# Performance work log

Hardware: AMD Instinct MI355X
Metric: run time of the kernel (lower is better)

The kernel has to match this reference:

```python
import jax, jax.numpy as jnp
import numpy as np
from jax import lax

EPS = 1e-5

def ste_sign(x):
    # forward-only module: plain sign is fine
    return jnp.sign(x)

def conv2d(x, w, pad):
    # x: NCHW, w: OIHW, stride 1
    return lax.conv_general_dilated(x, w, window_strides=(1, 1),
                                    padding=[(pad, pad), (pad, pad)],
                                    dimension_numbers=('NCHW', 'OIHW', 'NCHW'))

def maxpool2(x):
    # 2x2 max pool, stride 2, VALID (floor) -- matches nn.MaxPool2d(2,2)
    return lax.reduce_window(x, -jnp.inf, lax.max, (1, 1, 2, 2), (1, 1, 2, 2), 'VALID')

def batchnorm(x, gamma, beta):
    # training-mode BN: batch statistics over (N,H,W), biased variance
    mean = jnp.mean(x, axis=(0, 2, 3), keepdims=True)
    var = jnp.var(x, axis=(0, 2, 3), keepdims=True)
    xn = (x - mean) * lax.rsqrt(var + EPS)
    return xn * gamma[None, :, None, None] + beta[None, :, None, None]

def setup_inputs() -> dict:
    key = jax.random.key(0)
    ks = jax.random.split(key, 8)
    def he(k, shape):
        n = shape[2] * shape[3] * shape[0]
        return jax.random.normal(k, shape, jnp.float32) * np.sqrt(2.0 / n)
    x = jax.random.normal(ks[0], (4096, 1, 28, 28), jnp.float32)
    w0 = he(ks[1], (32, 1, 3, 3))
    w1 = he(ks[2], (32, 32, 3, 3))
    w2 = he(ks[3], (32, 32, 3, 3))
    g0 = jnp.ones((32,), jnp.float32); b0 = jnp.zeros((32,), jnp.float32)
    g1 = jnp.ones((32,), jnp.float32); b1 = jnp.zeros((32,), jnp.float32)
    g2 = jnp.ones((32,), jnp.float32); b2 = jnp.zeros((32,), jnp.float32)
    fw = jax.random.normal(ks[4], (10, 288), jnp.float32) * 0.01
    fb = jnp.zeros((10,), jnp.float32)
    return {"x": x, "w0": w0, "g0": g0, "b0": b0, "w1": w1, "g1": g1, "b1": b1,
            "w2": w2, "g2": g2, "b2": b2, "fw": fw, "fb": fb}

def reference(x, w0, g0, b0, w1, g1, b1, w2, g2, b2, fw, fb):
    # block0: fp conv -> pool -> bn (no act)
    h = batchnorm(maxpool2(conv2d(x, w0, 1)), g0, b0)          # [B,32,14,14]
    # block1: binary(1w1a) conv -> pool -> bn + maxpool(shortcut)
    o = batchnorm(maxpool2(conv2d(ste_sign(h), ste_sign(w1), 1)), g1, b1)
    h = o + maxpool2(h)                                         # [B,32,7,7]
    # block2
    o = batchnorm(maxpool2(conv2d(ste_sign(h), ste_sign(w2), 1)), g2, b2)
    h = o + maxpool2(h)                                         # [B,32,3,3]
    h = h.reshape(h.shape[0], -1)                                # [B,288]
    return h @ fw.T + fb                                         # [B,10]
```

## Files before the change

### kernel.cpp

```cpp
#include <hip/hip_runtime.h>
#include <stdint.h>

#define BATCH 4096

typedef float v16f __attribute__((ext_vector_type(16)));
typedef short v8s  __attribute__((ext_vector_type(8)));

__device__ __forceinline__ int sgn8(float v) {
    return (v > 0.f) ? 1 : ((v < 0.f) ? -1 : 0);
}

__global__ __launch_bounds__(448) void k_conv0s(const float* __restrict__ x,
                                                const float* __restrict__ w0,
                                                const float* __restrict__ w1,
                                                const float* __restrict__ w2,
                                                uint16_t* __restrict__ w1f,
                                                uint16_t* __restrict__ w2f,
                                                double* __restrict__ part0) {
    __shared__ float xs[960];
    __shared__ float wl[288];
    __shared__ double rs[448], rq[448];
    int n = blockIdx.x, t = threadIdx.x;

    if (n < 72 && t < 256) {
        int i = n * 256 + t;
        int ii = (i < 9216) ? i : i - 9216;
        const float* w = (i < 9216) ? w1 : w2;
        uint16_t* o = (i < 9216) ? w1f : w2f;
        int j = ii & 7, nn = (ii >> 3) & 31, q2 = (ii >> 8) & 1, kh = (ii >> 9) & 1, tp = ii >> 10;
        int cin = kh * 16 + q2 * 8 + j;
        float v = w[(nn * 32 + cin) * 9 + tp];
        o[ii] = (v > 0.f) ? 0x3F80 : ((v < 0.f) ? 0xBF80 : 0);
    }

    for (int i = t; i < 960; i += 448) xs[i] = 0.f;
    for (int i = t; i < 288; i += 448) wl[i] = w0[i];
    __syncthreads();
    for (int i = t; i < 784; i += 448) {
        int y = i / 28, xx = i - y * 28;
        xs[(y + 1) * 32 + xx + 1] = x[n * 784 + i];
    }
    __syncthreads();
    int c = t & 31, py = t >> 5;
    float wreg[9];
    #pragma unroll
    for (int i = 0; i < 9; ++i) wreg[i] = wl[c * 9 + i];
    const float4* X4 = (const float4*)xs;
    float4 cur0 = X4[(2 * py + 0) * 8];
    float4 cur1 = X4[(2 * py + 1) * 8];
    float4 cur2 = X4[(2 * py + 2) * 8];
    float4 cur3 = X4[(2 * py + 3) * 8];
    double s = 0.0, q = 0.0;
    #pragma unroll
    for (int k = 0; k < 7; ++k) {
        float4 n0 = X4[(2 * py + 0) * 8 + k + 1];
        float4 n1 = X4[(2 * py + 1) * 8 + k + 1];
        float4 n2 = X4[(2 * py + 2) * 8 + k + 1];
        float4 n3 = X4[(2 * py + 3) * 8 + k + 1];
        float a[4][6];
        a[0][0] = cur0.x; a[0][1] = cur0.y; a[0][2] = cur0.z; a[0][3] = cur0.w; a[0][4] = n0.x; a[0][5] = n0.y;
        a[1][0] = cur1.x; a[1][1] = cur1.y; a[1][2] = cur1.z; a[1][3] = cur1.w; a[1][4] = n1.x; a[1][5] = n1.y;
        a[2][0] = cur2.x; a[2][1] = cur2.y; a[2][2] = cur2.z; a[2][3] = cur2.w; a[2][4] = n2.x; a[2][5] = n2.y;
        a[3][0] = cur3.x; a[3][1] = cur3.y; a[3][2] = cur3.z; a[3][3] = cur3.w; a[3][4] = n3.x; a[3][5] = n3.y;
        #pragma unroll
        for (int e = 0; e < 2; ++e) {
            int base = 2 * e;
            float s00 = 0.f, s01 = 0.f, s10 = 0.f, s11 = 0.f;
            #pragma unroll
            for (int ky = 0; ky < 3; ++ky)
            #pragma unroll
            for (int kx = 0; kx < 3; ++kx) {
                float w = wreg[ky * 3 + kx];
                s00 = fmaf(a[ky][base + kx], w, s00);
                s01 = fmaf(a[ky][base + kx + 1], w, s01);
                s10 = fmaf(a[ky + 1][base + kx], w, s10);
                s11 = fmaf(a[ky + 1][base + kx + 1], w, s11);
            }
            float m = fmaxf(fmaxf(s00, s01), fmaxf(s10, s11));
            double v = (double)m;
            s += v; q += v * v;
        }
        cur0 = n0; cur1 = n1; cur2 = n2; cur3 = n3;
    }
    rs[c * 14 + py] = s; rq[c * 14 + py] = q;
    __syncthreads();
    if (t < 32) {
        double S = 0.0, Q = 0.0;
        #pragma unroll
        for (int i = 0; i < 14; ++i) { S += rs[t * 14 + i]; Q += rq[t * 14 + i]; }
        part0[(size_t)t * 4096 + n] = S;
        part0[(size_t)32 * 4096 + (size_t)t * 4096 + n] = Q;
    }
}

__global__ __launch_bounds__(256) void k_finalize(const double* __restrict__ part, int G,
                                                  const float* __restrict__ g,
                                                  const float* __restrict__ b,
                                                  double inv_count, float* __restrict__ ss) {
    int c = blockIdx.x, t = threadIdx.x;
    double s = 0.0, q = 0.0;
    for (int i = t; i < G; i += 256) {
        s += part[(size_t)c * G + i];
        q += part[(size_t)32 * G + (size_t)c * G + i];
    }
    #pragma unroll
    for (int o = 32; o > 0; o >>= 1) { s += __shfl_down(s, o); q += __shfl_down(q, o); }
    __shared__ double rs[4], rq[4];
    int w = t >> 6, l = t & 63;
    if (l == 0) { rs[w] = s; rq[w] = q; }
    __syncthreads();
    if (t == 0) {
        s = rs[0] + rs[1] + rs[2] + rs[3];
        q = rq[0] + rq[1] + rq[2] + rq[3];
        double mean = s * inv_count;
        double var = q * inv_count - mean * mean;
        double sc = (double)g[c] / sqrt(var + 1e-5);
        ss[c] = (float)sc;
        ss[32 + c] = (float)((double)b[c] - mean * sc);
    }
}

__global__ __launch_bounds__(448) void k_bn0r(const float* __restrict__ x,
                                              const float* __restrict__ w0,
                                              const float* __restrict__ ss,
                                              uint32_t* __restrict__ s0b,
                                              float* __restrict__ hp0) {
    __shared__ float xs[960];
    __shared__ float wl[288];
    __shared__ float P[6468];
    int n = blockIdx.x, t = threadIdx.x;
    for (int i = t; i < 960; i += 448) xs[i] = 0.f;
    for (int i = t; i < 288; i += 448) wl[i] = w0[i];
    __syncthreads();
    for (int i = t; i < 784; i += 448) {
        int y = i / 28, xx = i - y * 28;
        xs[(y + 1) * 32 + xx + 1] = x[n * 784 + i];
    }
    __syncthreads();
    int c = t & 31, py = t >> 5;
    float wreg[9];
    #pragma unroll
    for (int i = 0; i < 9; ++i) wreg[i] = wl[c * 9 + i];
    float sc = ss[c], sh = ss[32 + c];
    const float4* X4 = (const float4*)xs;
    float4 cur0 = X4[(2 * py + 0) * 8];
    float4 cur1 = X4[(2 * py + 1) * 8];
    float4 cur2 = X4[(2 * py + 2) * 8];
    float4 cur3 = X4[(2 * py + 3) * 8];
    #pragma unroll
    for (int k = 0; k < 7; ++k) {
        float4 n0 = X4[(2 * py + 0) * 8 + k + 1];
        float4 n1 = X4[(2 * py + 1) * 8 + k + 1];
        float4 n2 = X4[(2 * py + 2) * 8 + k + 1];
        float4 n3 = X4[(2 * py + 3) * 8 + k + 1];
        float a[4][6];
        a[0][0] = cur0.x; a[0][1] = cur0.y; a[0][2] = cur0.z; a[0][3] = cur0.w; a[0][4] = n0.x; a[0][5] = n0.y;
        a[1][0] = cur1.x; a[1][1] = cur1.y; a[1][2] = cur1.z; a[1][3] = cur1.w; a[1][4] = n1.x; a[1][5] = n1.y;
        a[2][0] = cur2.x; a[2][1] = cur2.y; a[2][2] = cur2.z; a[2][3] = cur2.w; a[2][4] = n2.x; a[2][5] = n2.y;
        a[3][0] = cur3.x; a[3][1] = cur3.y; a[3][2] = cur3.z; a[3][3] = cur3.w; a[3][4] = n3.x; a[3][5] = n3.y;
        #pragma unroll
        for (int e = 0; e < 2; ++e) {
            int base = 2 * e;
            float s00 = 0.f, s01 = 0.f, s10 = 0.f, s11 = 0.f;
            #pragma unroll
            for (int ky = 0; ky < 3; ++ky)
            #pragma unroll
            for (int kx = 0; kx < 3; ++kx) {
                float w = wreg[ky * 3 + kx];
                s00 = fmaf(a[ky][base + kx], w, s00);
                s01 = fmaf(a[ky][base + kx + 1], w, s01);
                s10 = fmaf(a[ky + 1][base + kx], w, s10);
                s11 = fmaf(a[ky + 1][base + kx + 1], w, s11);
            }
            float m = fmaxf(fmaxf(s00, s01), fmaxf(s10, s11));
            P[(py * 14 + 2 * k + e) * 33 + c] = fmaf(sc, m, sh);
        }
        cur0 = n0; cur1 = n1; cur2 = n2; cur3 = n3;
    }
    __syncthreads();
    uint32_t* simg = s0b + (size_t)n * 4096;
    for (int i = t; i < 784; i += 448) {
        int pl = i >> 2, qd = i & 3;
        int iy = pl / 14, ix = pl - iy * 14;
        int yy = iy + 1, xx2 = ix + 1;
        int p = yy * 16 + xx2;
        int psw = (xx2 & 3) ^ (yy & 3);
        int g = qd ^ psw;
        const float* Pp = &P[pl * 33 + g * 8];
        uint32_t d[4];
        #pragma unroll
        for (int j = 0; j < 4; ++j) {
            float h0 = Pp[2 * j], h1 = Pp[2 * j + 1];
            uint32_t b0 = (h0 > 0.f) ? 0x3F80u : ((h0 < 0.f) ? 0xBF80u : 0u);
            uint32_t b1 = (h1 > 0.f) ? 0x3F80u : ((h1 < 0.f) ? 0xBF80u : 0u);
            d[j] = b0 | (b1 << 16);
        }
        uint4 v; v.x = d[0]; v.y = d[1]; v.z = d[2]; v.w = d[3];
        *(uint4*)(simg + p * 16 + qd * 4) = v;
    }
    if (t < 240) {
        int e = t >> 2, qd = t & 3;
        int yh, xh;
        if (e < 16)      { yh = 0;      xh = e; }
        else if (e < 32) { yh = 15;     xh = e - 16; }
        else if (e < 46) { yh = e - 31; xh = 0; }
        else             { yh = e - 45; xh = 15; }
        uint4 z; z.x = z.y = z.z = z.w = 0u;
        *(uint4*)(simg + (yh * 16 + xh) * 16 + qd * 4) = z;
    }
    if (t < 196) {
        int pw = t >> 2, oct = t & 3;
        int pyy = pw / 7, pxx = pw - pyy * 7;
        int b00 = ((2 * pyy) * 14 + 2 * pxx) * 33;
        int b01 = b00 + 33;
        int b10 = b00 + 14 * 33;
        int b11 = b10 + 33;
        float out[8];
        #pragma unroll
        for (int k = 0; k < 8; ++k) {
            int cc = oct * 8 + k;
            out[k] = fmaxf(fmaxf(P[b00 + cc], P[b01 + cc]),
                           fmaxf(P[b10 + cc], P[b11 + cc]));
        }
        float4* hd = (float4*)(hp0 + ((size_t)n * 49 + pw) * 32 + oct * 8);
        float4 h0; h0.x = out[0]; h0.y = out[1]; h0.z = out[2]; h0.w = out[3];
        float4 h1; h1.x = out[4]; h1.y = out[5]; h1.z = out[6]; h1.w = out[7];
        hd[0] = h0; hd[1] = h1;
    }
}

__global__ __launch_bounds__(256) void k_conv1m(const uint32_t* __restrict__ s0b,
                                                const uint16_t* __restrict__ w1f,
                                                float* __restrict__ p1,
                                                double* __restrict__ part1) {
    __shared__ uint32_t lds[8192];
    int t = threadIdx.x;
    int n0 = blockIdx.x * 2;
    const uint4* gp = (const uint4*)(s0b + (size_t)n0 * 4096);
    uint4* lp = (uint4*)lds;
    #pragma unroll
    for (int i = 0; i < 8; ++i) lp[t + i * 256] = gp[t + i * 256];
    int lane = t & 63, wv = t >> 6;
    int q = lane >> 5, ncol = lane & 31;
    v8s wfr[18];
    #pragma unroll
    for (int f = 0; f < 18; ++f)
        wfr[f] = *(const v8s*)(w1f + (f * 2 + q) * 256 + ncol * 8);
    __syncthreads();
    int img = wv >> 1, wh = wv & 1;
    int n = n0 + img;
    int ibase = img * 4096;
    int m = lane & 31;
    int quad = m & 3, pwl = m >> 2;
    int dy = quad >> 1, dx = quad & 1;
    double sAcc = 0.0, qAcc = 0.0;
    for (int tile = wh; tile < 7; tile += 2) {
        int pw = tile * 8 + pwl;
        int pwc = min(pw, 48);
        int py = pwc / 7, px = pwc - py * 7;
        int pbase = (2 * py + dy) * 16 + 2 * px + dx;
        v16f acc;
        #pragma unroll
        for (int i = 0; i < 16; ++i) acc[i] = 0.f;
        #pragma unroll
        for (int tp = 0; tp < 9; ++tp) {
            int p = pbase + (tp / 3) * 16 + (tp % 3);
            int psw = (p ^ (p >> 4)) & 3;
            #pragma unroll
            for (int kh = 0; kh < 2; ++kh) {
                int g = kh * 2 + q;
                int idx = ibase + p * 16 + ((g ^ psw) << 2);
                v8s a = *(const v8s*)&lds[idx];
                acc = __builtin_amdgcn_mfma_f32_32x32x16_bf16(a, wfr[tp * 2 + kh], acc, 0, 0, 0);
            }
        }
        #pragma unroll
        for (int g4 = 0; g4 < 4; ++g4) {
            float mx = fmaxf(fmaxf(acc[4 * g4], acc[4 * g4 + 1]),
                             fmaxf(acc[4 * g4 + 2], acc[4 * g4 + 3]));
            int pwo = tile * 8 + 2 * g4 + q;
            if (pwo < 49) {
                p1[((size_t)n * 49 + pwo) * 32 + ncol] = mx;
                double v = (double)mx;
                sAcc += v; qAcc += v * v;
            }
        }
    }
    __syncthreads();
    double* red = (double*)lds;
    red[(wv * 2 + q) * 32 + ncol] = sAcc;
    red[256 + (wv * 2 + q) * 32 + ncol] = qAcc;
    __syncthreads();
    if (t < 32) {
        double S = 0.0, Q = 0.0;
        #pragma unroll
        for (int i = 0; i < 8; ++i) { S += red[i * 32 + t]; Q += red[256 + i * 32 + t]; }
        part1[(size_t)t * 2048 + blockIdx.x] = S;
        part1[(size_t)32 * 2048 + (size_t)t * 2048 + blockIdx.x] = Q;
    }
}

__global__ __launch_bounds__(256) void k_bc2m(const float* __restrict__ p1,
                                              const float* __restrict__ hp0,
                                              const float* __restrict__ ss,
                                              const uint16_t* __restrict__ w2f,
                                              float* __restrict__ p2,
                                              float* __restrict__ hp1,
                                              double* __restrict__ part2) {
    __shared__ uint32_t lds[8192];
    __shared__ float Htmp[1568];
    int t = threadIdx.x;
    int n0 = blockIdx.x * 8;
    int lane = t & 63, wv = t >> 6;
    int q = lane >> 5, ncol = lane & 31;
    v8s wfr[18];
    #pragma unroll
    for (int f = 0; f < 18; ++f)
        wfr[f] = *(const v8s*)(w2f + (f * 2 + q) * 256 + ncol * 8);

    int cbase = (t & 7) * 4;
    float sc4[4], sh4[4];
    #pragma unroll
    for (int j = 0; j < 4; ++j) { sc4[j] = ss[64 + cbase + j]; sh4[j] = ss[96 + cbase + j]; }

    float4 pa, pb, ha, hb;
    {
        const float4* P4 = (const float4*)(p1 + (size_t)n0 * 1568);
        const float4* H4 = (const float4*)(hp0 + (size_t)n0 * 1568);
        pa = P4[t]; ha = H4[t];
        if (t < 136) { pb = P4[256 + t]; hb = H4[256 + t]; }
    }

    float4* Ht4 = (float4*)Htmp;
    for (int img = 0; img < 8; ++img) {
        float4 npa, npb, nha, nhb;
        if (img < 7) {
            const float4* P4 = (const float4*)(p1 + (size_t)(n0 + img + 1) * 1568);
            const float4* H4 = (const float4*)(hp0 + (size_t)(n0 + img + 1) * 1568);
            npa = P4[t]; nha = H4[t];
            if (t < 136) { npb = P4[256 + t]; nhb = H4[256 + t]; }
        }
        if (img) __syncthreads();
        {
            float4 hv;
            hv.x = fmaf(sc4[0], pa.x, sh4[0]) + ha.x;
            hv.y = fmaf(sc4[1], pa.y, sh4[1]) + ha.y;
            hv.z = fmaf(sc4[2], pa.z, sh4[2]) + ha.z;
            hv.w = fmaf(sc4[3], pa.w, sh4[3]) + ha.w;
            Ht4[t] = hv;
            if (t < 136) {
                float4 hw;
                hw.x = fmaf(sc4[0], pb.x, sh4[0]) + hb.x;
                hw.y = fmaf(sc4[1], pb.y, sh4[1]) + hb.y;
                hw.z = fmaf(sc4[2], pb.z, sh4[2]) + hb.z;
                hw.w = fmaf(sc4[3], pb.w, sh4[3]) + hb.w;
                Ht4[256 + t] = hw;
            }
        }
        __syncthreads();
        uint32_t* ap = &lds[img * 1024];
        #pragma unroll
        for (int ii = 0; ii < 4; ++ii) {
            int i = t + ii * 256;
            int pp = i >> 4, r = i & 15;
            int y = pp >> 3, xq = pp & 7;
            uint32_t d = 0u;
            if (y >= 1 && xq >= 1) {
                int pix = (y - 1) * 7 + (xq - 1);
                int sub = r & 3;
                int g = (r >> 2) ^ (pp & 3);
                int c0 = ((g << 2) | sub) * 2;
                float h0 = Htmp[pix * 32 + c0];
                float h1 = Htmp[pix * 32 + c0 + 1];
                uint32_t b0 = (h0 > 0.f) ? 0x3F80u : ((h0 < 0.f) ? 0xBF80u : 0u);
                uint32_t b1 = (h1 > 0.f) ? 0x3F80u : ((h1 < 0.f) ? 0xBF80u : 0u);
                d = b0 | (b1 << 16);
            }
            ap[i] = d;
        }
        for (int jj = t; jj < 288; jj += 256) {
            int c = jj / 9, pix = jj - c * 9;
            int r = pix / 3, qq = pix - r * 3;
            float a0 = Htmp[((2 * r) * 7 + 2 * qq) * 32 + c];
            float a1 = Htmp[((2 * r) * 7 + 2 * qq + 1) * 32 + c];
            float a2 = Htmp[((2 * r + 1) * 7 + 2 * qq) * 32 + c];
            float a3 = Htmp[((2 * r + 1) * 7 + 2 * qq + 1) * 32 + c];
            hp1[(size_t)(n0 + img) * 288 + c * 9 + pix] = fmaxf(fmaxf(a0, a1), fmaxf(a2, a3));
        }
        pa = npa; pb = npb; ha = nha; hb = nhb;
    }
    __syncthreads();

    int m = lane & 31;
    int quad = m & 3, pwl = m >> 2;
    int dy = quad >> 1, dx = quad & 1;
    double sAcc = 0.0, qAcc = 0.0;
    for (int tile = wv; tile < 9; tile += 4) {
        int pwg = tile * 8 + pwl;
        int img = pwg / 9, pwi = pwg - img * 9;
        int py = pwi / 3, px = pwi - py * 3;
        int pbase = (2 * py + dy) * 8 + 2 * px + dx;
        v16f acc;
        #pragma unroll
        for (int i = 0; i < 16; ++i) acc[i] = 0.f;
        #pragma unroll
        for (int tp = 0; tp < 9; ++tp) {
            int p = pbase + (tp / 3) * 8 + (tp % 3);
            int psw = p & 3;
            #pragma unroll
            for (int kh = 0; kh < 2; ++kh) {
                int g = kh * 2 + q;
                int idx = img * 1024 + p * 16 + ((g ^ psw) << 2);
                v8s a = *(const v8s*)&lds[idx];
                acc = __builtin_amdgcn_mfma_f32_32x32x16_bf16(a, wfr[tp * 2 + kh], acc, 0, 0, 0);
            }
        }
        #pragma unroll
        for (int g4 = 0; g4 < 4; ++g4) {
            float mx = fmaxf(fmaxf(acc[4 * g4], acc[4 * g4 + 1]),
                             fmaxf(acc[4 * g4 + 2], acc[4 * g4 + 3]));
            int pwo = tile * 8 + 2 * g4 + q;
            int oimg = pwo / 9, opwi = pwo - oimg * 9;
            p2[(size_t)(n0 + oimg) * 288 + ncol * 9 + opwi] = mx;
            double v = (double)mx;
            sAcc += v; qAcc += v * v;
        }
    }
    __syncthreads();
    double* red = (double*)lds;
    red[(wv * 2 + q) * 32 + ncol] = sAcc;
    red[256 + (wv * 2 + q) * 32 + ncol] = qAcc;
    __syncthreads();
    if (t < 32) {
        double S = 0.0, Q = 0.0;
        #pragma unroll
        for (int i = 0; i < 8; ++i) { S += red[i * 32 + t]; Q += red[256 + i * 32 + t]; }
        part2[(size_t)t * 512 + blockIdx.x] = S;
        part2[(size_t)32 * 512 + (size_t)t * 512 + blockIdx.x] = Q;
    }
}

__global__ __launch_bounds__(256) void k_fc(const float* __restrict__ p2,
                                            const float* __restrict__ hp1,
                                            const float* __restrict__ ss,
                                            const float* __restrict__ fw,
                                            const float* __restrict__ fb,
                                            float* __restrict__ outv) {
    int wv = threadIdx.x >> 6, l = threadIdx.x & 63;
    int n = blockIdx.x * 4 + wv;
    float acc[10];
    #pragma unroll
    for (int k = 0; k < 10; ++k) acc[k] = 0.f;
    #pragma unroll
    for (int i = 0; i < 5; ++i) {
        int j = l + 64 * i;
        if (j < 288) {
            int c = j / 9;
            float h = fmaf(ss[128 + c], p2[n * 288 + j], ss[160 + c]) + hp1[n * 288 + j];
            #pragma unroll
            for (int k = 0; k < 10; ++k)
                acc[k] = fmaf(h, fw[k * 288 + j], acc[k]);
        }
    }
    #pragma unroll
    for (int k = 0; k < 10; ++k) {
        float s = acc[k];
        #pragma unroll
        for (int o = 32; o > 0; o >>= 1) s += __shfl_down(s, o);
        if (l == 0) outv[n * 10 + k] = s + fb[k];
    }
}

extern "C" void kernel_launch(void* const* d_in, const int* in_sizes, int n_in,
                              void* d_out, int out_size, void* d_ws, size_t ws_size,
                              hipStream_t stream) {
    (void)in_sizes; (void)n_in; (void)out_size; (void)ws_size;
    const float* x  = (const float*)d_in[0];
    const float* w0 = (const float*)d_in[1];
    const float* g0 = (const float*)d_in[2];
    const float* b0 = (const float*)d_in[3];
    const float* w1 = (const float*)d_in[4];
    const float* g1 = (const float*)d_in[5];
    const float* b1 = (const float*)d_in[6];
    const float* w2 = (const float*)d_in[7];
    const float* g2 = (const float*)d_in[8];
    const float* b2 = (const float*)d_in[9];
    const float* fw = (const float*)d_in[10];
    const float* fb = (const float*)d_in[11];
    float* outv = (float*)d_out;
    char* ws = (char*)d_ws;

    float*     ss    = (float*)(ws + 1024);
    uint16_t*  w1f   = (uint16_t*)(ws + 2048);
    uint16_t*  w2f   = (uint16_t*)(ws + 38912);
    float*     p1    = (float*)(ws + 76800);
    float*     hp1   = (float*)(ws + 32582656);
    float*     p2    = (float*)(ws + 37301248);
    uint32_t*  s0b   = (uint32_t*)(ws + 42019840);
    double*    part0 = (double*)(ws + 109128704);
    double*    part1 = (double*)(ws + 111225856);
    double*    part2 = (double*)(ws + 112274432);
    float*     hp0   = (float*)(ws + 128527360);

    k_conv0s<<<BATCH, 448, 0, stream>>>(x, w0, w1, w2, w1f, w2f, part0);
    k_finalize<<<32, 256, 0, stream>>>(part0, 4096, g0, b0, 1.0 / (BATCH * 196.0), ss);
    k_bn0r<<<BATCH, 448, 0, stream>>>(x, w0, ss, s0b, hp0);

    k_conv1m<<<BATCH / 2, 256, 0, stream>>>(s0b, w1f, p1, part1);
    k_finalize<<<32, 256, 0, stream>>>(part1, 2048, g1, b1, 1.0 / (BATCH * 49.0), ss + 64);

    k_bc2m<<<BATCH / 8, 256, 0, stream>>>(p1, hp0, ss, w2f, p2, hp1, part2);
    k_finalize<<<32, 256, 0, stream>>>(part2, 512, g2, b2, 1.0 / (BATCH * 9.0), ss + 128);

    k_fc<<<BATCH / 4, 256, 0, stream>>>(p2, hp1, ss, fw, fb, outv);
}
```

Baseline: 203.8 us.

## Store pooled conv0 output once and fold BN0 into downstream kernels

```diff
diff --git a/kernel.cpp b/kernel.cpp
--- a/kernel.cpp
+++ b/kernel.cpp
@@ -6,17 +6,14 @@
 typedef float v16f __attribute__((ext_vector_type(16)));
 typedef short v8s  __attribute__((ext_vector_type(8)));
 
-__device__ __forceinline__ int sgn8(float v) {
-    return (v > 0.f) ? 1 : ((v < 0.f) ? -1 : 0);
-}
-
-__global__ __launch_bounds__(448) void k_conv0s(const float* __restrict__ x,
+__global__ __launch_bounds__(448) void k_conv0f(const float* __restrict__ x,
                                                 const float* __restrict__ w0,
                                                 const float* __restrict__ w1,
                                                 const float* __restrict__ w2,
                                                 uint16_t* __restrict__ w1f,
                                                 uint16_t* __restrict__ w2f,
-                                                double* __restrict__ part0) {
+                                                double* __restrict__ part0,
+                                                float* __restrict__ mg) {
     __shared__ float xs[960];
     __shared__ float wl[288];
     __shared__ double rs[448], rq[448];
@@ -50,6 +47,7 @@
     float4 cur1 = X4[(2 * py + 1) * 8];
     float4 cur2 = X4[(2 * py + 2) * 8];
     float4 cur3 = X4[(2 * py + 3) * 8];
+    float* mrow = mg + (size_t)n * 6272;
     double s = 0.0, q = 0.0;
     #pragma unroll
     for (int k = 0; k < 7; ++k) {
@@ -77,6 +75,8 @@
                 s11 = fmaf(a[ky + 1][base + kx + 1], w, s11);
             }
             float m = fmaxf(fmaxf(s00, s01), fmaxf(s10, s11));
+            int pix = py * 14 + 2 * k + e;
+            mrow[pix * 32 + c] = m;
             double v = (double)m;
             s += v; q += v * v;
         }
@@ -120,138 +120,70 @@
     }
 }
 
-__global__ __launch_bounds__(448) void k_bn0r(const float* __restrict__ x,
-                                              const float* __restrict__ w0,
-                                              const float* __restrict__ ss,
-                                              uint32_t* __restrict__ s0b,
-                                              float* __restrict__ hp0) {
-    __shared__ float xs[960];
-    __shared__ float wl[288];
-    __shared__ float P[6468];
-    int n = blockIdx.x, t = threadIdx.x;
-    for (int i = t; i < 960; i += 448) xs[i] = 0.f;
-    for (int i = t; i < 288; i += 448) wl[i] = w0[i];
-    __syncthreads();
-    for (int i = t; i < 784; i += 448) {
-        int y = i / 28, xx = i - y * 28;
-        xs[(y + 1) * 32 + xx + 1] = x[n * 784 + i];
-    }
-    __syncthreads();
-    int c = t & 31, py = t >> 5;
-    float wreg[9];
-    #pragma unroll
-    for (int i = 0; i < 9; ++i) wreg[i] = wl[c * 9 + i];
-    float sc = ss[c], sh = ss[32 + c];
-    const float4* X4 = (const float4*)xs;
-    float4 cur0 = X4[(2 * py + 0) * 8];
-    float4 cur1 = X4[(2 * py + 1) * 8];
-    float4 cur2 = X4[(2 * py + 2) * 8];
-    float4 cur3 = X4[(2 * py + 3) * 8];
-    #pragma unroll
-    for (int k = 0; k < 7; ++k) {
-        float4 n0 = X4[(2 * py + 0) * 8 + k + 1];
-        float4 n1 = X4[(2 * py + 1) * 8 + k + 1];
-        float4 n2 = X4[(2 * py + 2) * 8 + k + 1];
-        float4 n3 = X4[(2 * py + 3) * 8 + k + 1];
-        float a[4][6];
-        a[0][0] = cur0.x; a[0][1] = cur0.y; a[0][2] = cur0.z; a[0][3] = cur0.w; a[0][4] = n0.x; a[0][5] = n0.y;
-        a[1][0] = cur1.x; a[1][1] = cur1.y; a[1][2] = cur1.z; a[1][3] = cur1.w; a[1][4] = n1.x; a[1][5] = n1.y;
-        a[2][0] = cur2.x; a[2][1] = cur2.y; a[2][2] = cur2.z; a[2][3] = cur2.w; a[2][4] = n2.x; a[2][5] = n2.y;
-        a[3][0] = cur3.x; a[3][1] = cur3.y; a[3][2] = cur3.z; a[3][3] = cur3.w; a[3][4] = n3.x; a[3][5] = n3.y;
-        #pragma unroll
-        for (int e = 0; e < 2; ++e) {
-            int base = 2 * e;
-            float s00 = 0.f, s01 = 0.f, s10 = 0.f, s11 = 0.f;
-            #pragma unroll
-            for (int ky = 0; ky < 3; ++ky)
-            #pragma unroll
-            for (int kx = 0; kx < 3; ++kx) {
-                float w = wreg[ky * 3 + kx];
-                s00 = fmaf(a[ky][base + kx], w, s00);
-                s01 = fmaf(a[ky][base + kx + 1], w, s01);
-                s10 = fmaf(a[ky + 1][base + kx], w, s10);
-                s11 = fmaf(a[ky + 1][base + kx + 1], w, s11);
-            }
-            float m = fmaxf(fmaxf(s00, s01), fmaxf(s10, s11));
-            P[(py * 14 + 2 * k + e) * 33 + c] = fmaf(sc, m, sh);
-        }
-        cur0 = n0; cur1 = n1; cur2 = n2; cur3 = n3;
-    }
-    __syncthreads();
-    uint32_t* simg = s0b + (size_t)n * 4096;
-    for (int i = t; i < 784; i += 448) {
-        int pl = i >> 2, qd = i & 3;
-        int iy = pl / 14, ix = pl - iy * 14;
-        int yy = iy + 1, xx2 = ix + 1;
-        int p = yy * 16 + xx2;
-        int psw = (xx2 & 3) ^ (yy & 3);
-        int g = qd ^ psw;
-        const float* Pp = &P[pl * 33 + g * 8];
-        uint32_t d[4];
-        #pragma unroll
-        for (int j = 0; j < 4; ++j) {
-            float h0 = Pp[2 * j], h1 = Pp[2 * j + 1];
-            uint32_t b0 = (h0 > 0.f) ? 0x3F80u : ((h0 < 0.f) ? 0xBF80u : 0u);
-            uint32_t b1 = (h1 > 0.f) ? 0x3F80u : ((h1 < 0.f) ? 0xBF80u : 0u);
-            d[j] = b0 | (b1 << 16);
-        }
-        uint4 v; v.x = d[0]; v.y = d[1]; v.z = d[2]; v.w = d[3];
-        *(uint4*)(simg + p * 16 + qd * 4) = v;
-    }
-    if (t < 240) {
-        int e = t >> 2, qd = t & 3;
-        int yh, xh;
-        if (e < 16)      { yh = 0;      xh = e; }
-        else if (e < 32) { yh = 15;     xh = e - 16; }
-        else if (e < 46) { yh = e - 31; xh = 0; }
-        else             { yh = e - 45; xh = 15; }
-        uint4 z; z.x = z.y = z.z = z.w = 0u;
-        *(uint4*)(simg + (yh * 16 + xh) * 16 + qd * 4) = z;
-    }
-    if (t < 196) {
-        int pw = t >> 2, oct = t & 3;
-        int pyy = pw / 7, pxx = pw - pyy * 7;
-        int b00 = ((2 * pyy) * 14 + 2 * pxx) * 33;
-        int b01 = b00 + 33;
-        int b10 = b00 + 14 * 33;
-        int b11 = b10 + 33;
-        float out[8];
-        #pragma unroll
-        for (int k = 0; k < 8; ++k) {
-            int cc = oct * 8 + k;
-            out[k] = fmaxf(fmaxf(P[b00 + cc], P[b01 + cc]),
-                           fmaxf(P[b10 + cc], P[b11 + cc]));
-        }
-        float4* hd = (float4*)(hp0 + ((size_t)n * 49 + pw) * 32 + oct * 8);
-        float4 h0; h0.x = out[0]; h0.y = out[1]; h0.z = out[2]; h0.w = out[3];
-        float4 h1; h1.x = out[4]; h1.y = out[5]; h1.z = out[6]; h1.w = out[7];
-        hd[0] = h0; hd[1] = h1;
-    }
-}
-
-__global__ __launch_bounds__(256) void k_conv1m(const uint32_t* __restrict__ s0b,
+__global__ __launch_bounds__(256) void k_conv1s(const float* __restrict__ m,
+                                                const float* __restrict__ ss,
                                                 const uint16_t* __restrict__ w1f,
                                                 float* __restrict__ p1,
                                                 double* __restrict__ part1) {
     __shared__ uint32_t lds[8192];
     int t = threadIdx.x;
     int n0 = blockIdx.x * 2;
-    const uint4* gp = (const uint4*)(s0b + (size_t)n0 * 4096);
-    uint4* lp = (uint4*)lds;
-    #pragma unroll
-    for (int i = 0; i < 8; ++i) lp[t + i * 256] = gp[t + i * 256];
     int lane = t & 63, wv = t >> 6;
     int q = lane >> 5, ncol = lane & 31;
     v8s wfr[18];
     #pragma unroll
     for (int f = 0; f < 18; ++f)
         wfr[f] = *(const v8s*)(w1f + (f * 2 + q) * 256 + ncol * 8);
-    __syncthreads();
+
+    uint4 z4; z4.x = z4.y = z4.z = z4.w = 0u;
+    for (int i = t; i < 480; i += 256) {
+        int img = (i >= 240) ? 1 : 0;
+        int e2 = i - img * 240;
+        int e = e2 >> 2, qd = e2 & 3;
+        int yh, xh;
+        if (e < 16)      { yh = 0;      xh = e; }
+        else if (e < 32) { yh = 15;     xh = e - 16; }
+        else if (e < 46) { yh = e - 31; xh = 0; }
+        else             { yh = e - 45; xh = 15; }
+        *(uint4*)&lds[img * 4096 + (yh * 16 + xh) * 16 + qd * 4] = z4;
+    }
+    int u = t >> 2, tq = t & 3;
+    float sc8[8], sh8[8];
+    #pragma unroll
+    for (int j = 0; j < 8; ++j) { sc8[j] = ss[tq * 8 + j]; sh8[j] = ss[32 + tq * 8 + j]; }
+    for (int pg = u; pg < 392; pg += 64) {
+        int img = (pg >= 196) ? 1 : 0;
+        int pl = pg - img * 196;
+        int iy = pl / 14, ix = pl - iy * 14;
+        int yy = iy + 1, xx2 = ix + 1;
+        int p = yy * 16 + xx2;
+        int psw = (xx2 & 3) ^ (yy & 3);
+        int qd = tq ^ psw;
+        const float4* mp = (const float4*)(m + ((size_t)(n0 + img) * 196 + pl) * 32 + tq * 8);
+        float4 v0 = mp[0], v1 = mp[1];
+        float h[8];
+        h[0] = fmaf(sc8[0], v0.x, sh8[0]); h[1] = fmaf(sc8[1], v0.y, sh8[1]);
+        h[2] = fmaf(sc8[2], v0.z, sh8[2]); h[3] = fmaf(sc8[3], v0.w, sh8[3]);
+        h[4] = fmaf(sc8[4], v1.x, sh8[4]); h[5] = fmaf(sc8[5], v1.y, sh8[5]);
+        h[6] = fmaf(sc8[6], v1.z, sh8[6]); h[7] = fmaf(sc8[7], v1.w, sh8[7]);
+        uint32_t d[4];
+        #pragma unroll
+        for (int j = 0; j < 4; ++j) {
+            float h0 = h[2 * j], h1 = h[2 * j + 1];
+            uint32_t b0 = (h0 > 0.f) ? 0x3F80u : ((h0 < 0.f) ? 0xBF80u : 0u);
+            uint32_t b1 = (h1 > 0.f) ? 0x3F80u : ((h1 < 0.f) ? 0xBF80u : 0u);
+            d[j] = b0 | (b1 << 16);
+        }
+        uint4 v; v.x = d[0]; v.y = d[1]; v.z = d[2]; v.w = d[3];
+        *(uint4*)&lds[img * 4096 + p * 16 + qd * 4] = v;
+    }
+    __syncthreads();
+
     int img = wv >> 1, wh = wv & 1;
     int n = n0 + img;
     int ibase = img * 4096;
-    int m = lane & 31;
-    int quad = m & 3, pwl = m >> 2;
+    int mm = lane & 31;
+    int quad = mm & 3, pwl = mm >> 2;
     int dy = quad >> 1, dx = quad & 1;
     double sAcc = 0.0, qAcc = 0.0;
     for (int tile = wh; tile < 7; tile += 2) {
@@ -301,7 +233,7 @@
 }
 
 __global__ __launch_bounds__(256) void k_bc2m(const float* __restrict__ p1,
-                                              const float* __restrict__ hp0,
+                                              const float* __restrict__ m,
                                               const float* __restrict__ ss,
                                               const uint16_t* __restrict__ w2f,
                                               float* __restrict__ p2,
@@ -313,47 +245,84 @@
     int n0 = blockIdx.x * 8;
     int lane = t & 63, wv = t >> 6;
     int q = lane >> 5, ncol = lane & 31;
-    v8s wfr[18];
-    #pragma unroll
-    for (int f = 0; f < 18; ++f)
-        wfr[f] = *(const v8s*)(w2f + (f * 2 + q) * 256 + ncol * 8);
-
-    int cbase = (t & 7) * 4;
-    float sc4[4], sh4[4];
-    #pragma unroll
-    for (int j = 0; j < 4; ++j) { sc4[j] = ss[64 + cbase + j]; sh4[j] = ss[96 + cbase + j]; }
-
-    float4 pa, pb, ha, hb;
+
+    int cb = t & 7;
+    float sc1v[4], sh1v[4], sc0v[4], sh0v[4];
+    #pragma unroll
+    for (int j = 0; j < 4; ++j) {
+        sc1v[j] = ss[64 + cb * 4 + j]; sh1v[j] = ss[96 + cb * 4 + j];
+        sc0v[j] = ss[cb * 4 + j];      sh0v[j] = ss[32 + cb * 4 + j];
+    }
+    int pw0 = t >> 3;
+    int py0 = pw0 / 7, px0 = pw0 - py0 * 7;
+    int mb0 = ((2 * py0) * 14 + 2 * px0) * 8 + cb;
+    int pw1 = 32 + (t >> 3);
+    int py1 = pw1 / 7, px1 = pw1 - py1 * 7;
+    int mb1 = ((2 * py1) * 14 + 2 * px1) * 8 + cb;
+
+    float4 pa, pb, a0, a1, a2, a3, b0_, b1_, b2_, b3_;
     {
         const float4* P4 = (const float4*)(p1 + (size_t)n0 * 1568);
-        const float4* H4 = (const float4*)(hp0 + (size_t)n0 * 1568);
-        pa = P4[t]; ha = H4[t];
-        if (t < 136) { pb = P4[256 + t]; hb = H4[256 + t]; }
+        const float4* M4 = (const float4*)(m + (size_t)n0 * 6272);
+        pa = P4[t];
+        a0 = M4[mb0]; a1 = M4[mb0 + 8]; a2 = M4[mb0 + 112]; a3 = M4[mb0 + 120];
+        if (t < 136) {
+            pb = P4[256 + t];
+            b0_ = M4[mb1]; b1_ = M4[mb1 + 8]; b2_ = M4[mb1 + 112]; b3_ = M4[mb1 + 120];
+        }
     }
 
     float4* Ht4 = (float4*)Htmp;
     for (int img = 0; img < 8; ++img) {
-        float4 npa, npb, nha, nhb;
+        float4 npa, npb, na0, na1, na2, na3, nb0, nb1, nb2, nb3;
         if (img < 7) {
             const float4* P4 = (const float4*)(p1 + (size_t)(n0 + img + 1) * 1568);
-            const float4* H4 = (const float4*)(hp0 + (size_t)(n0 + img + 1) * 1568);
-            npa = P4[t]; nha = H4[t];
-            if (t < 136) { npb = P4[256 + t]; nhb = H4[256 + t]; }
+            const float4* M4 = (const float4*)(m + (size_t)(n0 + img + 1) * 6272);
+            npa = P4[t];
+            na0 = M4[mb0]; na1 = M4[mb0 + 8]; na2 = M4[mb0 + 112]; na3 = M4[mb0 + 120];
+            if (t < 136) {
+                npb = P4[256 + t];
+                nb0 = M4[mb1]; nb1 = M4[mb1 + 8]; nb2 = M4[mb1 + 112]; nb3 = M4[mb1 + 120];
+            }
         }
         if (img) __syncthreads();
         {
+            float mx0 = fmaxf(fmaxf(a0.x, a1.x), fmaxf(a2.x, a3.x));
+            float mx1 = fmaxf(fmaxf(a0.y, a1.y), fmaxf(a2.y, a3.y));
+            float mx2 = fmaxf(fmaxf(a0.z, a1.z), fmaxf(a2.z, a3.z));
+            float mx3 = fmaxf(fmaxf(a0.w, a1.w), fmaxf(a2.w, a3.w));
+            float mn0 = fminf(fminf(a0.x, a1.x), fminf(a2.x, a3.x));
+            float mn1 = fminf(fminf(a0.y, a1.y), fminf(a2.y, a3.y));
+            float mn2 = fminf(fminf(a0.z, a1.z), fminf(a2.z, a3.z));
+            float mn3 = fminf(fminf(a0.w, a1.w), fminf(a2.w, a3.w));
+            float s0 = (sc0v[0] > 0.f) ? mx0 : mn0;
+            float s1 = (sc0v[1] > 0.f) ? mx1 : mn1;
+            float s2 = (sc0v[2] > 0.f) ? mx2 : mn2;
+            float s3 = (sc0v[3] > 0.f) ? mx3 : mn3;
             float4 hv;
-            hv.x = fmaf(sc4[0], pa.x, sh4[0]) + ha.x;
-            hv.y = fmaf(sc4[1], pa.y, sh4[1]) + ha.y;
-            hv.z = fmaf(sc4[2], pa.z, sh4[2]) + ha.z;
-            hv.w = fmaf(sc4[3], pa.w, sh4[3]) + ha.w;
+            hv.x = fmaf(sc1v[0], pa.x, sh1v[0]) + fmaf(sc0v[0], s0, sh0v[0]);
+            hv.y = fmaf(sc1v[1], pa.y, sh1v[1]) + fmaf(sc0v[1], s1, sh0v[1]);
+            hv.z = fmaf(sc1v[2], pa.z, sh1v[2]) + fmaf(sc0v[2], s2, sh0v[2]);
+            hv.w = fmaf(sc1v[3], pa.w, sh1v[3]) + fmaf(sc0v[3], s3, sh0v[3]);
             Ht4[t] = hv;
             if (t < 136) {
+                float ux0 = fmaxf(fmaxf(b0_.x, b1_.x), fmaxf(b2_.x, b3_.x));
+                float ux1 = fmaxf(fmaxf(b0_.y, b1_.y), fmaxf(b2_.y, b3_.y));
+                float ux2 = fmaxf(fmaxf(b0_.z, b1_.z), fmaxf(b2_.z, b3_.z));
+                float ux3 = fmaxf(fmaxf(b0_.w, b1_.w), fmaxf(b2_.w, b3_.w));
+                float un0 = fminf(fminf(b0_.x, b1_.x), fminf(b2_.x, b3_.x));
+                float un1 = fminf(fminf(b0_.y, b1_.y), fminf(b2_.y, b3_.y));
+                float un2 = fminf(fminf(b0_.z, b1_.z), fminf(b2_.z, b3_.z));
+                float un3 = fminf(fminf(b0_.w, b1_.w), fminf(b2_.w, b3_.w));
+                float u0 = (sc0v[0] > 0.f) ? ux0 : un0;
+                float u1 = (sc0v[1] > 0.f) ? ux1 : un1;
+                float u2 = (sc0v[2] > 0.f) ? ux2 : un2;
+                float u3 = (sc0v[3] > 0.f) ? ux3 : un3;
                 float4 hw;
-                hw.x = fmaf(sc4[0], pb.x, sh4[0]) + hb.x;
-                hw.y = fmaf(sc4[1], pb.y, sh4[1]) + hb.y;
-                hw.z = fmaf(sc4[2], pb.z, sh4[2]) + hb.z;
-                hw.w = fmaf(sc4[3], pb.w, sh4[3]) + hb.w;
+                hw.x = fmaf(sc1v[0], pb.x, sh1v[0]) + fmaf(sc0v[0], u0, sh0v[0]);
+                hw.y = fmaf(sc1v[1], pb.y, sh1v[1]) + fmaf(sc0v[1], u1, sh0v[1]);
+                hw.z = fmaf(sc1v[2], pb.z, sh1v[2]) + fmaf(sc0v[2], u2, sh0v[2]);
+                hw.w = fmaf(sc1v[3], pb.w, sh1v[3]) + fmaf(sc0v[3], u3, sh0v[3]);
                 Ht4[256 + t] = hw;
             }
         }
@@ -372,27 +341,34 @@
                 int c0 = ((g << 2) | sub) * 2;
                 float h0 = Htmp[pix * 32 + c0];
                 float h1 = Htmp[pix * 32 + c0 + 1];
-                uint32_t b0 = (h0 > 0.f) ? 0x3F80u : ((h0 < 0.f) ? 0xBF80u : 0u);
-                uint32_t b1 = (h1 > 0.f) ? 0x3F80u : ((h1 < 0.f) ? 0xBF80u : 0u);
-                d = b0 | (b1 << 16);
+                uint32_t w0b = (h0 > 0.f) ? 0x3F80u : ((h0 < 0.f) ? 0xBF80u : 0u);
+                uint32_t w1b = (h1 > 0.f) ? 0x3F80u : ((h1 < 0.f) ? 0xBF80u : 0u);
+                d = w0b | (w1b << 16);
             }
             ap[i] = d;
         }
         for (int jj = t; jj < 288; jj += 256) {
             int c = jj / 9, pix = jj - c * 9;
             int r = pix / 3, qq = pix - r * 3;
-            float a0 = Htmp[((2 * r) * 7 + 2 * qq) * 32 + c];
-            float a1 = Htmp[((2 * r) * 7 + 2 * qq + 1) * 32 + c];
-            float a2 = Htmp[((2 * r + 1) * 7 + 2 * qq) * 32 + c];
-            float a3 = Htmp[((2 * r + 1) * 7 + 2 * qq + 1) * 32 + c];
-            hp1[(size_t)(n0 + img) * 288 + c * 9 + pix] = fmaxf(fmaxf(a0, a1), fmaxf(a2, a3));
-        }
-        pa = npa; pb = npb; ha = nha; hb = nhb;
-    }
-    __syncthreads();
-
-    int m = lane & 31;
-    int quad = m & 3, pwl = m >> 2;
+            float e0 = Htmp[((2 * r) * 7 + 2 * qq) * 32 + c];
+            float e1 = Htmp[((2 * r) * 7 + 2 * qq + 1) * 32 + c];
+            float e2 = Htmp[((2 * r + 1) * 7 + 2 * qq) * 32 + c];
+            float e3 = Htmp[((2 * r + 1) * 7 + 2 * qq + 1) * 32 + c];
+            hp1[(size_t)(n0 + img) * 288 + c * 9 + pix] = fmaxf(fmaxf(e0, e1), fmaxf(e2, e3));
+        }
+        pa = npa; pb = npb;
+        a0 = na0; a1 = na1; a2 = na2; a3 = na3;
+        b0_ = nb0; b1_ = nb1; b2_ = nb2; b3_ = nb3;
+    }
+    __syncthreads();
+
+    v8s wfr[18];
+    #pragma unroll
+    for (int f = 0; f < 18; ++f)
+        wfr[f] = *(const v8s*)(w2f + (f * 2 + q) * 256 + ncol * 8);
+
+    int mmm = lane & 31;
+    int quad = mmm & 3, pwl = mmm >> 2;
     int dy = quad >> 1, dx = quad & 1;
     double sAcc = 0.0, qAcc = 0.0;
     for (int tile = wv; tile < 9; tile += 4) {
@@ -492,24 +468,22 @@
 
     float*     ss    = (float*)(ws + 1024);
     uint16_t*  w1f   = (uint16_t*)(ws + 2048);
-    uint16_t*  w2f   = (uint16_t*)(ws + 38912);
-    float*     p1    = (float*)(ws + 76800);
-    float*     hp1   = (float*)(ws + 32582656);
-    float*     p2    = (float*)(ws + 37301248);
-    uint32_t*  s0b   = (uint32_t*)(ws + 42019840);
-    double*    part0 = (double*)(ws + 109128704);
-    double*    part1 = (double*)(ws + 111225856);
-    double*    part2 = (double*)(ws + 112274432);
-    float*     hp0   = (float*)(ws + 128527360);
-
-    k_conv0s<<<BATCH, 448, 0, stream>>>(x, w0, w1, w2, w1f, w2f, part0);
+    uint16_t*  w2f   = (uint16_t*)(ws + 20480);
+    double*    part1 = (double*)(ws + 38912);
+    double*    part0 = (double*)(ws + 1087488);
+    float*     p1    = (float*)(ws + 3184640);
+    float*     p2    = (float*)(ws + 28874752);
+    float*     hp1   = (float*)(ws + 33593344);
+    double*    part2 = (double*)(ws + 38311936);
+    float*     m     = (float*)(ws + 38574080);
+
+    k_conv0f<<<BATCH, 448, 0, stream>>>(x, w0, w1, w2, w1f, w2f, part0, m);
     k_finalize<<<32, 256, 0, stream>>>(part0, 4096, g0, b0, 1.0 / (BATCH * 196.0), ss);
-    k_bn0r<<<BATCH, 448, 0, stream>>>(x, w0, ss, s0b, hp0);
-
-    k_conv1m<<<BATCH / 2, 256, 0, stream>>>(s0b, w1f, p1, part1);
+
+    k_conv1s<<<BATCH / 2, 256, 0, stream>>>(m, ss, w1f, p1, part1);
     k_finalize<<<32, 256, 0, stream>>>(part1, 2048, g1, b1, 1.0 / (BATCH * 49.0), ss + 64);
 
-    k_bc2m<<<BATCH / 8, 256, 0, stream>>>(p1, hp0, ss, w2f, p2, hp1, part2);
+    k_bc2m<<<BATCH / 8, 256, 0, stream>>>(p1, m, ss, w2f, p2, hp1, part2);
     k_finalize<<<32, 256, 0, stream>>>(part2, 512, g2, b2, 1.0 / (BATCH * 9.0), ss + 128);
 
     k_fc<<<BATCH / 4, 256, 0, stream>>>(p2, hp1, ss, fw, fb, outv);
```

New measurement: 185.9 us. 1.1x faster.
